# Performance work log

Measured on AMD Instinct MI355X. Metric: run time of the kernel, lower is better.

Reference implementation:

```python
import jax, jax.numpy as jnp
import numpy as np

B, S, D, H, O, E, K = 8, 2048, 768, 3072, 768, 8, 2
LN_EPS = 1e-5


def setup_inputs() -> dict:
    key = jax.random.key(0)
    ks = jax.random.split(key, 8)
    x = jax.random.normal(ks[0], (B, S, D), dtype=jnp.float32)
    router_w = jax.random.normal(ks[1], (D, E), dtype=jnp.float32) * 0.02
    router_b = jnp.zeros((E,), dtype=jnp.float32)
    w1 = jax.random.normal(ks[2], (E, D, H), dtype=jnp.float32) * 0.02
    b1 = jnp.zeros((E, H), dtype=jnp.float32)
    w2 = jax.random.normal(ks[3], (E, H, O), dtype=jnp.float32) * 0.02
    b2 = jnp.zeros((E, O), dtype=jnp.float32)
    ln_g = jnp.ones((O,), dtype=jnp.float32)
    ln_b = jnp.zeros((O,), dtype=jnp.float32)
    return {"x": x, "router_w": router_w, "router_b": router_b,
            "w1": w1, "b1": b1, "w2": w2, "b2": b2,
            "ln_g": ln_g, "ln_b": ln_b}


def _layernorm(y, g, b):
    mu = jnp.mean(y, axis=-1, keepdims=True)
    var = jnp.mean(jnp.square(y - mu), axis=-1, keepdims=True)
    return (y - mu) * jax.lax.rsqrt(var + LN_EPS) * g + b


def reference(x, router_w, router_b, w1, b1, w2, b2, ln_g, ln_b):
    # Router (NoisyTopKRouter, eval mode: no noise): top-k gate over expert logits
    logits = jnp.einsum('bsd,de->bse', x, router_w) + router_b   # [B,S,E]
    top_vals, top_idx = jax.lax.top_k(logits, K)                 # [B,S,K]
    routing_weights = jax.nn.softmax(top_vals, axis=-1)          # [B,S,K]

    out = jnp.zeros((B, S, O), dtype=x.dtype)
    for e in range(E):
        # per-token combined weight for this expert (0 if not routed)
        w_e = jnp.sum(routing_weights * (top_idx == e), axis=-1)  # [B,S]
        # dense per-expert feedforward on ALL tokens (as in original loop)
        h = jax.nn.gelu(jnp.einsum('bsd,dh->bsh', x, w1[e]) + b1[e])
        y = jnp.einsum('bsh,ho->bso', h, w2[e]) + b2[e]
        out = out + y * w_e[..., None]
    return _layernorm(out, ln_g, ln_b)
```

## Files before the change

### kernel.cpp

```cpp
#include <hip/hip_runtime.h>
#include <hip/hip_bf16.h>
#include <stdint.h>

#define Bq  8
#define Sq  2048
#define Dq  768
#define Hq  3072
#define Oq  768
#define Eq  8
#define Mq  (Bq*Sq)
#define LN_EPS 1e-5f
#define MAX_T256 (Mq/128 + 16)

typedef unsigned short u16;
typedef __attribute__((ext_vector_type(4))) float f32x4;
typedef __attribute__((ext_vector_type(8))) __bf16 bf16x8;

static __device__ __forceinline__ u16 f2bf(float f) {
  __hip_bfloat16 h = __float2bfloat16(f);
  return __builtin_bit_cast(u16, h);
}

static __device__ __forceinline__ float gelu_f(float x) {
  float u = 0.7978845608028654f * x * (1.0f + 0.044715f * x * x);
  float e = __expf(2.0f * u);
  float t = 1.0f - 2.0f / (e + 1.0f);
  return 0.5f * x * (1.0f + t);
}

typedef const __attribute__((address_space(1))) void* gas_t;
typedef __attribute__((address_space(3))) void* las_t;
static __device__ __forceinline__ void gload16(const void* g, void* l) {
  __builtin_amdgcn_global_load_lds((gas_t)g, (las_t)l, 16, 0, 0);
}

__global__ __launch_bounds__(256) void router_cvt_kernel(
    const float* __restrict__ x, const float* __restrict__ rw,
    const float* __restrict__ rb, u16* __restrict__ Xbf,
    int* __restrict__ tok_seg, float2* __restrict__ tok_w)
{
  __shared__ float rwT[Eq * Dq];
  for (int i = threadIdx.x; i < Eq * Dq; i += 256)
    rwT[(i & 7) * Dq + (i >> 3)] = rw[i];
  __syncthreads();

  int wid = threadIdx.x >> 6;
  int lane = threadIdx.x & 63;
  int token = blockIdx.x * 4 + wid;
  const float4* xrow = (const float4*)(x + (size_t)token * Dq);
  ushort4* orow = (ushort4*)(Xbf + (size_t)token * Dq);

  float acc[Eq];
#pragma unroll
  for (int e = 0; e < Eq; e++) acc[e] = 0.f;

#pragma unroll
  for (int it = 0; it < Dq / 256; it++) {
    int d4 = it * 64 + lane;
    float4 xv = xrow[d4];
    ushort4 o;
    o.x = f2bf(xv.x); o.y = f2bf(xv.y); o.z = f2bf(xv.z); o.w = f2bf(xv.w);
    orow[d4] = o;
    int d = d4 * 4;
#pragma unroll
    for (int e = 0; e < Eq; e++) {
      float4 wv = *(const float4*)&rwT[e * Dq + d];
      acc[e] += xv.x * wv.x + xv.y * wv.y + xv.z * wv.z + xv.w * wv.w;
    }
  }
#pragma unroll
  for (int e = 0; e < Eq; e++) {
    float v = acc[e];
#pragma unroll
    for (int off = 32; off; off >>= 1) v += __shfl_xor(v, off);
    acc[e] = v;
  }
  if (lane == 0) {
    float v1 = -1e30f, v2 = -1e30f; int i1 = 0, i2 = 0;
#pragma unroll
    for (int e = 0; e < Eq; e++) {
      float v = acc[e] + rb[e];
      if (v > v1)      { v2 = v1; i2 = i1; v1 = v; i1 = e; }
      else if (v > v2) { v2 = v;  i2 = e; }
    }
    float ex = expf(v2 - v1);
    float wa = 1.f / (1.f + ex);
    float wb = ex / (1.f + ex);
    tok_seg[token] = i1 | ((8 + i2) << 8);
    tok_w[token] = make_float2(wa, wb);
  }
}

__global__ __launch_bounds__(256) void scatter_build(
    const int* __restrict__ tok_seg, const float2* __restrict__ tok_w,
    int* __restrict__ cnt, int* __restrict__ seg_tok, float* __restrict__ seg_wgt)
{
  __shared__ int histA[16], histB[16], base[16];
  int t = threadIdx.x;
  if (t < 16) { histA[t] = 0; histB[t] = 0; }
  __syncthreads();
  int token = blockIdx.x * 256 + t;
  int sp = tok_seg[token];
  float2 wv = tok_w[token];
  int s0 = sp & 0xff, s1 = sp >> 8;
  atomicAdd(&histA[s0], 1);
  atomicAdd(&histA[s1], 1);
  __syncthreads();
  if (t < 16) base[t] = atomicAdd(&cnt[t], histA[t]);
  __syncthreads();
  int p0 = base[s0] + atomicAdd(&histB[s0], 1);
  seg_tok[(size_t)s0 * Mq + p0] = token;
  seg_wgt[(size_t)s0 * Mq + p0] = wv.x;
  int p1 = base[s1] + atomicAdd(&histB[s1], 1);
  seg_tok[(size_t)s1 * Mq + p1] = token;
  seg_wgt[(size_t)s1 * Mq + p1] = wv.y;
}

__global__ void prefix_kernel(const int* __restrict__ cnt, int* __restrict__ prefix)
{
  if (threadIdx.x == 0 && blockIdx.x == 0) {
    int t = 0;
#pragma unroll
    for (int s = 0; s < 16; s++) { prefix[s] = t; t += (cnt[s] + 255) >> 8; }
    prefix[16] = t;
  }
}

__global__ __launch_bounds__(256) void transpose_cvt(
    const float* __restrict__ in, u16* __restrict__ out, int R, int C)
{
  __shared__ float tile[32][33];
  int e = blockIdx.z;
  in  += (size_t)e * R * C;
  out += (size_t)e * R * C;
  int c0 = blockIdx.x * 32, r0 = blockIdx.y * 32;
  int tx = threadIdx.x & 31, ty = threadIdx.x >> 5;
#pragma unroll
  for (int rr = 0; rr < 32; rr += 8)
    tile[rr + ty][tx] = in[(size_t)(r0 + rr + ty) * C + c0 + tx];
  __syncthreads();
#pragma unroll
  for (int rr = 0; rr < 32; rr += 8)
    out[(size_t)(c0 + rr + ty) * R + r0 + tx] = f2bf(tile[tx][rr + ty]);
}

__global__ __launch_bounds__(512, 2) void moe_gemm1(
    const u16* __restrict__ A, const u16* __restrict__ W,
    const float* __restrict__ bias, u16* __restrict__ Hout,
    const int* __restrict__ cnt, const int* __restrict__ prefix,
    const int* __restrict__ seg_tok, int K, int N, int tile_lo)
{
  const int NP = N / 256;
  const int lid = (int)blockIdx.x + NP * (int)blockIdx.y;
  const int xcd = lid & 7, slot = lid >> 3;
  const int t_loc = xcd + 8 * (slot / NP);
  const int panel = slot % NP;

  const int t = tile_lo + t_loc;
  if (t >= prefix[16]) return;
  int seg = 0;
#pragma unroll
  for (int s = 1; s < 16; s++) if (prefix[s] <= t) seg = s;
  const int e = seg & 7;
  const int segcnt = cnt[seg];
  const int ti = t - prefix[seg];
  const int lt = t_loc;

  __shared__ u16 smem[65536];
  const int tid  = threadIdx.x;
  const int lane = tid & 63;
  const int wid  = tid >> 6;
  const int wr   = wid >> 2, wc = wid & 3;
  const int lrow = lane & 15, kgrp = lane >> 4;
  const int gcx0 = ((kgrp)     ^ (lrow & 7)) * 8;
  const int gcx1 = ((4 + kgrp) ^ (lrow & 7)) * 8;

  f32x4 acc[8][4];
#pragma unroll
  for (int m = 0; m < 8; m++)
#pragma unroll
    for (int n = 0; n < 4; n++) acc[m][n] = (f32x4){0.f, 0.f, 0.f, 0.f};

  const int srow = tid >> 3;
  const int swz  = ((tid & 7) ^ (srow & 7)) * 8;
  const u16 *pA00, *pA01, *pA10, *pA11, *pB00, *pB01, *pB10, *pB11;
  {
    int sr;
    sr = ti * 256 +   0 +  0 + srow;
    pA00 = A + (size_t)((sr < segcnt) ? seg_tok[(size_t)seg * Mq + sr] : 0) * K + swz;
    sr = ti * 256 +   0 + 64 + srow;
    pA01 = A + (size_t)((sr < segcnt) ? seg_tok[(size_t)seg * Mq + sr] : 0) * K + swz;
    sr = ti * 256 + 128 +  0 + srow;
    pA10 = A + (size_t)((sr < segcnt) ? seg_tok[(size_t)seg * Mq + sr] : 0) * K + swz;
    sr = ti * 256 + 128 + 64 + srow;
    pA11 = A + (size_t)((sr < segcnt) ? seg_tok[(size_t)seg * Mq + sr] : 0) * K + swz;
    const u16* Wb = W + (size_t)e * K * N;
    pB00 = Wb + (size_t)(panel * 256 +   0 +  0 + srow) * K + swz;
    pB01 = Wb + (size_t)(panel * 256 +   0 + 64 + srow) * K + swz;
    pB10 = Wb + (size_t)(panel * 256 + 128 +  0 + srow) * K + swz;
    pB11 = Wb + (size_t)(panel * 256 + 128 + 64 + srow) * K + swz;
  }

#define STG(base, h, P0, P1)                               \
  do {                                                     \
    gload16(P0, &smem[(base) + (h) * 8192 + tid * 8]);     \
    gload16(P1, &smem[(base) + (h) * 8192 + 4096 + tid * 8]); \
    P0 += 64; P1 += 64;                                    \
  } while (0)

  const int NKT = K / 64;
  STG(0, 0, pA00, pA01); STG(0, 1, pA10, pA11);
  STG(32768, 0, pB00, pB01); STG(32768, 1, pB10, pB11);

  bf16x8 bfr[4][2];
  for (int kt = 0; kt < NKT; ++kt) {
    const int s = kt & 1;
    const int sA = s * 16384, sB = 32768 + s * 16384;
    const int dA = (s ^ 1) * 16384, dB = 32768 + (s ^ 1) * 16384;
    const bool more = (kt + 1 < NKT);
    const int abase = wr * 128 + lrow;
    const int bbase = wc * 64 + lrow;

    if (more) {
      STG(dA, 0, pA00, pA01);
      asm volatile("s_waitcnt vmcnt(2)" ::: "memory");
    } else {
      asm volatile("s_waitcnt vmcnt(0)" ::: "memory");
    }
    __builtin_amdgcn_s_barrier();
    __builtin_amdgcn_sched_barrier(0);
#pragma unroll
    for (int n = 0; n < 4; n++) {
      bfr[n][0] = *(const bf16x8*)&smem[sB + (bbase + n * 16) * 64 + gcx0];
      bfr[n][1] = *(const bf16x8*)&smem[sB + (bbase + n * 16) * 64 + gcx1];
    }
    {
      bf16x8 a00 = *(const bf16x8*)&smem[sA + (abase +  0) * 64 + gcx0];
      bf16x8 a01 = *(const bf16x8*)&smem[sA + (abase +  0) * 64 + gcx1];
      bf16x8 a10 = *(const bf16x8*)&smem[sA + (abase + 16) * 64 + gcx0];
      bf16x8 a11 = *(const bf16x8*)&smem[sA + (abase + 16) * 64 + gcx1];
      __builtin_amdgcn_s_setprio(1);
#pragma unroll
      for (int n = 0; n < 4; n++) {
        acc[0][n] = __builtin_amdgcn_mfma_f32_16x16x32_bf16(a00, bfr[n][0], acc[0][n], 0, 0, 0);
        acc[0][n] = __builtin_amdgcn_mfma_f32_16x16x32_bf16(a01, bfr[n][1], acc[0][n], 0, 0, 0);
        acc[1][n] = __builtin_amdgcn_mfma_f32_16x16x32_bf16(a10, bfr[n][0], acc[1][n], 0, 0, 0);
        acc[1][n] = __builtin_amdgcn_mfma_f32_16x16x32_bf16(a11, bfr[n][1], acc[1][n], 0, 0, 0);
      }
      __builtin_amdgcn_s_setprio(0);
    }
    __builtin_amdgcn_sched_barrier(0);
    __builtin_amdgcn_s_barrier();

#define PHASE(q, STGSTMT)                                                     \
    do {                                                                      \
      bf16x8 a00 = *(const bf16x8*)&smem[sA + (abase + (2*(q))    * 16) * 64 + gcx0]; \
      bf16x8 a01 = *(const bf16x8*)&smem[sA + (abase + (2*(q))    * 16) * 64 + gcx1]; \
      bf16x8 a10 = *(const bf16x8*)&smem[sA + (abase + (2*(q)+1)  * 16) * 64 + gcx0]; \
      bf16x8 a11 = *(const bf16x8*)&smem[sA + (abase + (2*(q)+1)  * 16) * 64 + gcx1]; \
      if (more) { STGSTMT; }                                                  \
      __builtin_amdgcn_s_setprio(1);                                          \
      _Pragma("unroll")                                                       \
      for (int n = 0; n < 4; n++) {                                           \
        acc[2*(q)][n]   = __builtin_amdgcn_mfma_f32_16x16x32_bf16(a00, bfr[n][0], acc[2*(q)][n], 0, 0, 0);   \
        acc[2*(q)][n]   = __builtin_amdgcn_mfma_f32_16x16x32_bf16(a01, bfr[n][1], acc[2*(q)][n], 0, 0, 0);   \
        acc[2*(q)+1][n] = __builtin_amdgcn_mfma_f32_16x16x32_bf16(a10, bfr[n][0], acc[2*(q)+1][n], 0, 0, 0); \
        acc[2*(q)+1][n] = __builtin_amdgcn_mfma_f32_16x16x32_bf16(a11, bfr[n][1], acc[2*(q)+1][n], 0, 0, 0); \
      }                                                                       \
      __builtin_amdgcn_s_setprio(0);                                          \
      __builtin_amdgcn_sched_barrier(0);                                      \
      __builtin_amdgcn_s_barrier();                                           \
    } while (0)

    PHASE(1, STG(dA, 1, pA10, pA11));
    PHASE(2, STG(dB, 0, pB00, pB01));
    PHASE(3, STG(dB, 1, pB10, pB11));
#undef PHASE
  }
#undef STG

  {
    const int rb = wr * 128, cb = wc * 64;
#pragma unroll
    for (int n = 0; n < 4; n++) {
      int cc = cb + n * 16 + lrow;
      float bv = bias[(size_t)e * N + panel * 256 + cc];
#pragma unroll
      for (int m = 0; m < 8; m++)
#pragma unroll
        for (int j = 0; j < 4; j++) {
          int rr = rb + m * 16 + kgrp * 4 + j;
          smem[rr * 256 + cc] = f2bf(gelu_f(acc[m][n][j] + bv));
        }
    }
    __syncthreads();
    const int r = tid >> 5, c8 = (tid & 31) * 8;
    u16* gdst = Hout + (size_t)(lt * 256) * N + (size_t)panel * 256;
#pragma unroll
    for (int it2 = 0; it2 < 16; ++it2) {
      int rr = it2 * 16 + r;
      *(uint4*)(gdst + (size_t)rr * N + c8) = *(const uint4*)&smem[rr * 256 + c8];
    }
  }
}

__global__ __launch_bounds__(256) void moe_gemm2(
    const u16* __restrict__ A, const u16* __restrict__ W,
    const float* __restrict__ bias, float* __restrict__ out,
    const int* __restrict__ cnt, const int* __restrict__ prefix,
    const int* __restrict__ seg_tok, const float* __restrict__ seg_wgt,
    int K, int N, int tile_lo)
{
  const int NP = N / 128;
  const int lid = (int)blockIdx.x + NP * (int)blockIdx.y;
  const int xcd = lid & 7, slot = lid >> 3;
  const int t2 = xcd + 8 * (slot / NP);
  const int panel = slot % NP;

  const int t256 = tile_lo + (t2 >> 1);
  if (t256 >= prefix[16]) return;
  int seg = 0;
#pragma unroll
  for (int s = 1; s < 16; s++) if (prefix[s] <= t256) seg = s;
  const int e = seg & 7;
  const int segcnt = cnt[seg];
  const int ti = (t256 - prefix[seg]) * 2 + (t2 & 1);
  const int lt = t2;

  __shared__ u16 As[2][128 * 32];
  __shared__ u16 Bs[2][128 * 32];
  const int tid  = threadIdx.x;
  const int lane = tid & 63;
  const int wid  = tid >> 6;
  const int wr   = wid >> 1, wc = wid & 1;
  const int lrow = lane & 15, kgrp = lane >> 4;
  const int kx   = kgrp ^ ((lrow >> 1) & 3);
  const int n0 = panel * 128;

  f32x4 acc[4][4];
#pragma unroll
  for (int m = 0; m < 4; m++)
#pragma unroll
    for (int n = 0; n < 4; n++) acc[m][n] = (f32x4){0.f, 0.f, 0.f, 0.f};

  const int r0 = tid >> 2;
  const int kc = (((tid & 3) ^ ((tid >> 3) & 3)) * 8);
  const u16* gA0 = A + (size_t)(lt * 128 + r0) * K + kc;
  const u16* gA1 = gA0 + (size_t)64 * K;
  const u16* gB = W + (size_t)e * K * N + (size_t)(n0 + r0) * K + kc;
  const size_t rowskipB = (size_t)64 * K;
  const int lofs = tid * 8;

  auto stage = [&](int b) {
    gload16(gA0, &As[b][lofs]);
    gload16(gA1, &As[b][lofs + 2048]);
    gload16(gB,            &Bs[b][lofs]);
    gload16(gB + rowskipB, &Bs[b][lofs + 2048]);
    gA0 += 32; gA1 += 32; gB += 32;
  };

  const int NIT = K / 32;
  stage(0);
  for (int it = 0; it < NIT; ++it) {
    const int cur = it & 1;
    if (it + 1 < NIT) {
      stage(cur ^ 1);
      asm volatile("s_waitcnt vmcnt(4)" ::: "memory");
    } else {
      asm volatile("s_waitcnt vmcnt(0)" ::: "memory");
    }
    __builtin_amdgcn_s_barrier();
    __builtin_amdgcn_sched_barrier(0);
    bf16x8 a[4], b[4];
#pragma unroll
    for (int m = 0; m < 4; m++)
      a[m] = *(const bf16x8*)&As[cur][(wr * 64 + m * 16 + lrow) * 32 + kx * 8];
#pragma unroll
    for (int n = 0; n < 4; n++)
      b[n] = *(const bf16x8*)&Bs[cur][(wc * 64 + n * 16 + lrow) * 32 + kx * 8];
#pragma unroll
    for (int m = 0; m < 4; m++)
#pragma unroll
      for (int n = 0; n < 4; n++)
        acc[m][n] = __builtin_amdgcn_mfma_f32_16x16x32_bf16(a[m], b[n], acc[m][n], 0, 0, 0);
    __builtin_amdgcn_sched_barrier(0);
    __builtin_amdgcn_s_barrier();
  }

  const int rbase = wr * 64;
  const int cbase = n0 + wc * 64;
#pragma unroll
  for (int m = 0; m < 4; m++)
#pragma unroll
    for (int j = 0; j < 4; j++) {
      int r = rbase + m * 16 + kgrp * 4 + j;
      int i = ti * 128 + r;
      if (i < segcnt) {
        int token = seg_tok[(size_t)seg * Mq + i];
        float w = seg_wgt[(size_t)seg * Mq + i];
        float* orow = out + (size_t)token * Oq;
#pragma unroll
        for (int n = 0; n < 4; n++) {
          int c = cbase + n * 16 + lrow;
          float v = (acc[m][n][j] + bias[(size_t)e * N + c]) * w;
          unsafeAtomicAdd(&orow[c], v);
        }
      }
    }
}

__global__ __launch_bounds__(256) void ln_kernel(
    float* __restrict__ io, const float* __restrict__ g, const float* __restrict__ b)
{
  int wid = threadIdx.x >> 6, lane = threadIdx.x & 63;
  int row = blockIdx.x * 4 + wid;
  float* p = io + (size_t)row * Oq;
  float v[Oq / 64];
  float s = 0.f;
#pragma unroll
  for (int i = 0; i < Oq / 64; i++) { v[i] = p[lane + i * 64]; s += v[i]; }
#pragma unroll
  for (int off = 32; off; off >>= 1) s += __shfl_xor(s, off);
  float mu = s * (1.0f / Oq);
  float q = 0.f;
#pragma unroll
  for (int i = 0; i < Oq / 64; i++) { float d = v[i] - mu; q += d * d; }
#pragma unroll
  for (int off = 32; off; off >>= 1) q += __shfl_xor(q, off);
  float inv = rsqrtf(q * (1.0f / Oq) + LN_EPS);
#pragma unroll
  for (int i = 0; i < Oq / 64; i++) {
    int c = lane + i * 64;
    p[c] = (v[i] - mu) * inv * g[c] + b[c];
  }
}

extern "C" void kernel_launch(void* const* d_in, const int* in_sizes, int n_in,
                              void* d_out, int out_size, void* d_ws, size_t ws_size,
                              hipStream_t stream)
{
  const float* x    = (const float*)d_in[0];
  const float* rw   = (const float*)d_in[1];
  const float* rb   = (const float*)d_in[2];
  const float* w1   = (const float*)d_in[3];
  const float* b1   = (const float*)d_in[4];
  const float* w2   = (const float*)d_in[5];
  const float* b2   = (const float*)d_in[6];
  const float* ln_g = (const float*)d_in[7];
  const float* ln_b = (const float*)d_in[8];
  float* out = (float*)d_out;

  char* ws = (char*)d_ws;
  size_t off = 0;
  auto alloc = [&](size_t bytes) {
    void* p = ws + off;
    off += (bytes + 255) & ~(size_t)255;
    return p;
  };
  int*    cnt     = (int*)alloc(16 * 4);
  int*    prefix  = (int*)alloc(17 * 4);
  int*    tok_seg = (int*)alloc((size_t)Mq * 4);
  float2* tok_w   = (float2*)alloc((size_t)Mq * 8);
  int*    seg_tok = (int*)alloc((size_t)16 * Mq * 4);
  float*  seg_wgt = (float*)alloc((size_t)16 * Mq * 4);
  u16* Xbf = (u16*)alloc((size_t)Mq * Dq * 2);
  u16* W1T = (u16*)alloc((size_t)Eq * Dq * Hq * 2);
  u16* W2T = (u16*)alloc((size_t)Eq * Hq * Oq * 2);

  size_t remain = (ws_size > off) ? ws_size - off : 0;
  size_t tile_bytes = (size_t)256 * Hq * 2;
  long long wt = (long long)(remain / tile_bytes);
  if (wt > MAX_T256) wt = MAX_T256;
  wt &= ~7LL;
  if (wt < 8) wt = 8;
  int WT = (int)wt;
  u16* Hbuf = (u16*)alloc((size_t)WT * tile_bytes);

  hipMemsetAsync(out, 0, (size_t)Mq * Oq * 4, stream);
  hipMemsetAsync(cnt, 0, 16 * 4, stream);
  router_cvt_kernel<<<Mq / 4, 256, 0, stream>>>(x, rw, rb, Xbf, tok_seg, tok_w);
  scatter_build<<<Mq / 256, 256, 0, stream>>>(tok_seg, tok_w, cnt, seg_tok, seg_wgt);
  prefix_kernel<<<1, 64, 0, stream>>>(cnt, prefix);
  transpose_cvt<<<dim3(Hq / 32, Dq / 32, Eq), 256, 0, stream>>>(w1, W1T, Dq, Hq);
  transpose_cvt<<<dim3(Oq / 32, Hq / 32, Eq), 256, 0, stream>>>(w2, W2T, Hq, Oq);

  for (int tl = 0; tl < MAX_T256; tl += WT) {
    int gx = MAX_T256 - tl; if (gx > WT) gx = WT;
    moe_gemm1<<<dim3(Hq / 256, gx), 512, 0, stream>>>(
        Xbf, W1T, b1, Hbuf, cnt, prefix, seg_tok, Dq, Hq, tl);
    moe_gemm2<<<dim3(Oq / 128, 2 * gx), 256, 0, stream>>>(
        Hbuf, W2T, b2, out, cnt, prefix, seg_tok, seg_wgt, Hq, Oq, tl);
  }
  ln_kernel<<<Mq / 4, 256, 0, stream>>>(out, ln_g, ln_b);
}
```

Measured before the change: 735.5 us.

## Deepen second GEMM K-tile to 64 with 8-way swizzle, set MFMA priority, vectorize LN

```diff
diff --git a/kernel.cpp b/kernel.cpp
--- a/kernel.cpp
+++ b/kernel.cpp
@@ -327,14 +327,15 @@
   const int ti = (t256 - prefix[seg]) * 2 + (t2 & 1);
   const int lt = t2;
 
-  __shared__ u16 As[2][128 * 32];
-  __shared__ u16 Bs[2][128 * 32];
+  __shared__ u16 As[2][128 * 64];
+  __shared__ u16 Bs[2][128 * 64];
   const int tid  = threadIdx.x;
   const int lane = tid & 63;
   const int wid  = tid >> 6;
   const int wr   = wid >> 1, wc = wid & 1;
   const int lrow = lane & 15, kgrp = lane >> 4;
-  const int kx   = kgrp ^ ((lrow >> 1) & 3);
+  const int cx0  = ((kgrp)     ^ (lrow & 7)) * 8;
+  const int cx1  = ((4 + kgrp) ^ (lrow & 7)) * 8;
   const int n0 = panel * 128;
 
   f32x4 acc[4][4];
@@ -343,46 +344,63 @@
 #pragma unroll
     for (int n = 0; n < 4; n++) acc[m][n] = (f32x4){0.f, 0.f, 0.f, 0.f};
 
-  const int r0 = tid >> 2;
-  const int kc = (((tid & 3) ^ ((tid >> 3) & 3)) * 8);
-  const u16* gA0 = A + (size_t)(lt * 128 + r0) * K + kc;
-  const u16* gA1 = gA0 + (size_t)64 * K;
-  const u16* gB = W + (size_t)e * K * N + (size_t)(n0 + r0) * K + kc;
-  const size_t rowskipB = (size_t)64 * K;
-  const int lofs = tid * 8;
+  const int srow = tid >> 3;
+  const int swz  = ((tid & 7) ^ (srow & 7)) * 8;
+  const u16* gA[4];
+  const u16* gB[4];
+#pragma unroll
+  for (int c = 0; c < 4; c++) {
+    gA[c] = A + (size_t)(lt * 128 + c * 32 + srow) * K + swz;
+    gB[c] = W + (size_t)e * K * N + (size_t)(n0 + c * 32 + srow) * K + swz;
+  }
 
   auto stage = [&](int b) {
-    gload16(gA0, &As[b][lofs]);
-    gload16(gA1, &As[b][lofs + 2048]);
-    gload16(gB,            &Bs[b][lofs]);
-    gload16(gB + rowskipB, &Bs[b][lofs + 2048]);
-    gA0 += 32; gA1 += 32; gB += 32;
+#pragma unroll
+    for (int c = 0; c < 4; c++) {
+      gload16(gA[c], &As[b][(c * 32 + srow) * 64 + (tid & 7) * 8]);
+      gA[c] += 64;
+    }
+#pragma unroll
+    for (int c = 0; c < 4; c++) {
+      gload16(gB[c], &Bs[b][(c * 32 + srow) * 64 + (tid & 7) * 8]);
+      gB[c] += 64;
+    }
   };
 
-  const int NIT = K / 32;
+  const int NIT = K / 64;
   stage(0);
   for (int it = 0; it < NIT; ++it) {
     const int cur = it & 1;
     if (it + 1 < NIT) {
       stage(cur ^ 1);
-      asm volatile("s_waitcnt vmcnt(4)" ::: "memory");
+      asm volatile("s_waitcnt vmcnt(8)" ::: "memory");
     } else {
       asm volatile("s_waitcnt vmcnt(0)" ::: "memory");
     }
     __builtin_amdgcn_s_barrier();
     __builtin_amdgcn_sched_barrier(0);
-    bf16x8 a[4], b[4];
+    bf16x8 a[4][2], b[4][2];
+#pragma unroll
+    for (int m = 0; m < 4; m++) {
+      int row = wr * 64 + m * 16 + lrow;
+      a[m][0] = *(const bf16x8*)&As[cur][row * 64 + cx0];
+      a[m][1] = *(const bf16x8*)&As[cur][row * 64 + cx1];
+    }
+#pragma unroll
+    for (int n = 0; n < 4; n++) {
+      int row = wc * 64 + n * 16 + lrow;
+      b[n][0] = *(const bf16x8*)&Bs[cur][row * 64 + cx0];
+      b[n][1] = *(const bf16x8*)&Bs[cur][row * 64 + cx1];
+    }
+    __builtin_amdgcn_s_setprio(1);
 #pragma unroll
     for (int m = 0; m < 4; m++)
-      a[m] = *(const bf16x8*)&As[cur][(wr * 64 + m * 16 + lrow) * 32 + kx * 8];
-#pragma unroll
-    for (int n = 0; n < 4; n++)
-      b[n] = *(const bf16x8*)&Bs[cur][(wc * 64 + n * 16 + lrow) * 32 + kx * 8];
-#pragma unroll
-    for (int m = 0; m < 4; m++)
-#pragma unroll
-      for (int n = 0; n < 4; n++)
-        acc[m][n] = __builtin_amdgcn_mfma_f32_16x16x32_bf16(a[m], b[n], acc[m][n], 0, 0, 0);
+#pragma unroll
+      for (int n = 0; n < 4; n++) {
+        acc[m][n] = __builtin_amdgcn_mfma_f32_16x16x32_bf16(a[m][0], b[n][0], acc[m][n], 0, 0, 0);
+        acc[m][n] = __builtin_amdgcn_mfma_f32_16x16x32_bf16(a[m][1], b[n][1], acc[m][n], 0, 0, 0);
+      }
+    __builtin_amdgcn_s_setprio(0);
     __builtin_amdgcn_sched_barrier(0);
     __builtin_amdgcn_s_barrier();
   }
@@ -414,24 +432,37 @@
 {
   int wid = threadIdx.x >> 6, lane = threadIdx.x & 63;
   int row = blockIdx.x * 4 + wid;
-  float* p = io + (size_t)row * Oq;
-  float v[Oq / 64];
+  float4* p = (float4*)(io + (size_t)row * Oq);
+  float4 v[3];
   float s = 0.f;
 #pragma unroll
-  for (int i = 0; i < Oq / 64; i++) { v[i] = p[lane + i * 64]; s += v[i]; }
+  for (int i = 0; i < 3; i++) {
+    v[i] = p[lane + i * 64];
+    s += v[i].x + v[i].y + v[i].z + v[i].w;
+  }
 #pragma unroll
   for (int off = 32; off; off >>= 1) s += __shfl_xor(s, off);
   float mu = s * (1.0f / Oq);
   float q = 0.f;
 #pragma unroll
-  for (int i = 0; i < Oq / 64; i++) { float d = v[i] - mu; q += d * d; }
+  for (int i = 0; i < 3; i++) {
+    float d0 = v[i].x - mu, d1 = v[i].y - mu, d2 = v[i].z - mu, d3 = v[i].w - mu;
+    q += d0 * d0 + d1 * d1 + d2 * d2 + d3 * d3;
+  }
 #pragma unroll
   for (int off = 32; off; off >>= 1) q += __shfl_xor(q, off);
   float inv = rsqrtf(q * (1.0f / Oq) + LN_EPS);
 #pragma unroll
-  for (int i = 0; i < Oq / 64; i++) {
-    int c = lane + i * 64;
-    p[c] = (v[i] - mu) * inv * g[c] + b[c];
+  for (int i = 0; i < 3; i++) {
+    int c = (lane + i * 64) * 4;
+    float4 gv = *(const float4*)(g + c);
+    float4 bv = *(const float4*)(b + c);
+    float4 o;
+    o.x = (v[i].x - mu) * inv * gv.x + bv.x;
+    o.y = (v[i].y - mu) * inv * gv.y + bv.y;
+    o.z = (v[i].z - mu) * inv * gv.z + bv.z;
+    o.w = (v[i].w - mu) * inv * gv.w + bv.w;
+    p[lane + i * 64] = o;
   }
 }
 
```

Measured after the change: 758.1 us. 3.1% more time.
